# Optimization experiments

Hardware: AMD Instinct MI355X
Metric: run time of the kernel (lower is better)

Reference implementation:

```python
import jax, jax.numpy as jnp
import numpy as np

N_NODES = 50000
NB = 32          # neighbor-list width per metapath
NFEAT = 128
NHID = 64
DIM_MP = 64
EDIM = 32
NMETA = 3
NCLASS = 8
B = 10000
ALPHA = 0.2


def setup_inputs() -> dict:
    key = jax.random.key(0)
    ks = jax.random.split(key, 16)
    s = 0.05
    return {
        "input": jax.random.normal(ks[0], (B, NFEAT), jnp.float32),
        "index": jax.random.randint(ks[1], (B,), 0, N_NODES),
        "node_emb": jax.random.normal(ks[2], (N_NODES, NFEAT), jnp.float32),
        "edge_index": jax.random.randint(ks[3], (NMETA, N_NODES, NB), 0, N_NODES, dtype=jnp.int32),
        "edge_emb": jax.random.normal(ks[4], (NMETA, N_NODES * NB, EDIM), jnp.float32) * 0.1,
        "n_sample": 32,
        "Wq1": jax.random.normal(ks[5], (NMETA, NFEAT, NHID), jnp.float32) * s,
        "Wk1": jax.random.normal(ks[6], (NMETA, NFEAT, NHID), jnp.float32) * s,
        "a1": jax.random.normal(ks[7], (NMETA, 2 * NHID + EDIM), jnp.float32) * s,
        "Wq2": jax.random.normal(ks[8], (NMETA, NHID, DIM_MP), jnp.float32) * s,
        "Wk2": jax.random.normal(ks[9], (NMETA, NFEAT, DIM_MP), jnp.float32) * s,
        "a2": jax.random.normal(ks[10], (NMETA, 2 * DIM_MP + EDIM), jnp.float32) * s,
        "a_mp": jax.random.normal(ks[11], (DIM_MP,), jnp.float32) * s,
        "Wc": jax.random.normal(ks[12], (DIM_MP, NCLASS), jnp.float32) * s,
        "bc": jnp.zeros((NCLASS,), jnp.float32),
    }


def _aggr(x, index, node_emb, nbr_tab, e_tab, Wq, Wk, a, out_dim, n_sample):
    """GAT-style edge-embedding attention aggregation over sampled neighbors.
    x:[B,in]  nbr_tab:[N,NB] int  e_tab:[N,NB,E]
    """
    nbrs = nbr_tab[index][:, :n_sample]              # [B,S] gathered neighbor ids
    e_emb = e_tab[index][:, :n_sample]               # [B,S,E] per-edge embeddings
    hq = x @ Wq                                      # [B,out]
    hk = node_emb[nbrs] @ Wk                         # [B,S,out] (irregular gather + GEMM)
    # attention score: a^T [hq || hk || e_ij]
    scores = (hq @ a[:out_dim])[:, None] + hk @ a[out_dim:2 * out_dim] + e_emb @ a[2 * out_dim:]
    scores = jax.nn.leaky_relu(scores, ALPHA)        # [B,S]
    att = jax.nn.softmax(scores, axis=1)
    agg = jnp.einsum('bs,bso->bo', att, hk)          # scatter-weighted aggregation
    return jax.nn.elu(agg)


def reference(input, index, node_emb, edge_index, edge_emb,
              Wq1, Wk1, a1, Wq2, Wk2, a2, a_mp, Wc, bc, n_sample):
    embs = []
    for m in range(NMETA):  # fixed small metapath loop (structurally distinct params)
        nbr_tab = edge_index[m]                              # [N,NB]
        e_tab = edge_emb[m].reshape(N_NODES, NB, EDIM)       # [N,NB,E]
        x1 = _aggr(input, index, node_emb, nbr_tab, e_tab, Wq1[m], Wk1[m], a1[m], NHID, n_sample)
        x2 = _aggr(x1, index, node_emb, nbr_tab, e_tab, Wq2[m], Wk2[m], a2[m], DIM_MP, n_sample)
        embs.append(x2)
    emb = jnp.stack(embs)                                    # [M,B,R]
    # metapath-level attention fusion
    e = jax.nn.leaky_relu(emb @ a_mp, ALPHA)                 # [M,B]
    att = jax.nn.softmax(e, axis=0)
    fused = jnp.einsum('mb,mbr->br', att, emb)               # [B,R]
    logits = jax.nn.relu(fused @ Wc + bc)                    # [B,nclass]
    return jax.nn.log_softmax(logits, axis=1)
```

## Files before the change

### kernel.cpp

```cpp
#include <hip/hip_runtime.h>
#include <hip/hip_bf16.h>
#include <cstddef>

#define NNODES 50000
#define NBW    32
#define NFEAT  128
#define NHID   64
#define EDIM   32
#define NMETA  3
#define NCLASS 8
#define BB     10000
#define SS     32

#define OFF_HKA   9600000
#define OFF_WQ1V  9900000
#define OFF_WQ2V  9900384
#define OFF_WBF   9900576

#define NGEMMBLK  782

typedef __attribute__((ext_vector_type(8))) short bf16x8;
typedef __attribute__((ext_vector_type(4))) float f32x4;

static __device__ __forceinline__ unsigned short f2bf(float x) {
    unsigned u = __float_as_uint(x);
    return (unsigned short)((u + 0x7fffu + ((u >> 16) & 1u)) >> 16);
}
static __device__ __forceinline__ float rdlane_f(float v, int l) {
    return __int_as_float(__builtin_amdgcn_readlane(__float_as_int(v), l));
}

__global__ void prep_kernel(const float* __restrict__ Wq1, const float* __restrict__ a1,
                            const float* __restrict__ Wq2, const float* __restrict__ a2,
                            const float* __restrict__ Wk1, const float* __restrict__ Wk2,
                            float* __restrict__ wq1v, float* __restrict__ wq2v,
                            unsigned short* __restrict__ Bf)
{
    int blk = blockIdx.x, t = threadIdx.x;
    if (blk < 24) {
        int id = blk * 256 + t;
        int lane = id & 63;
        int t4 = (id >> 6) & 3;
        int kk = (id >> 8) & 3;
        int mat = id >> 10;
        const float* W = (mat < 3) ? (Wk1 + (size_t)mat * 8192)
                                   : (Wk2 + (size_t)(mat - 3) * 8192);
        int c  = t4 * 16 + (lane & 15);
        int kb = kk * 32 + (lane >> 4) * 8;
        unsigned short* dst = Bf + (size_t)id * 8;
        #pragma unroll
        for (int j = 0; j < 8; ++j) dst[j] = f2bf(W[(size_t)(kb + j) * 64 + c]);
    } else {
        int m = blk - 24;
        if (t < 128) {
            float acc = 0.f;
            const float* w = Wq1 + (m * 128 + t) * 64;
            const float* a = a1 + m * 160;
            #pragma unroll 8
            for (int c = 0; c < 64; ++c) acc += w[c] * a[c];
            wq1v[m * 128 + t] = acc;
        } else if (t < 192) {
            int f = t - 128;
            float acc = 0.f;
            const float* w = Wq2 + (m * 64 + f) * 64;
            const float* a = a2 + m * 160;
            #pragma unroll 8
            for (int c = 0; c < 64; ++c) acc += w[c] * a[c];
            wq2v[m * 64 + f] = acc;
        }
    }
}

__global__ __launch_bounds__(256) void hk_mfma6(const float* __restrict__ node_emb,
                                                const unsigned short* __restrict__ Bf,
                                                const float* __restrict__ a1,
                                                const float* __restrict__ a2,
                                                unsigned* __restrict__ HKI,
                                                float* __restrict__ hkaI)
{
    __shared__ char lds_a[64 * 256];
    int nbase = blockIdx.x * 64;
    int t = threadIdx.x;

    #pragma unroll
    for (int i = 0; i < 8; ++i) {
        int fi = (i * 256 + t) * 4;
        int row = fi >> 7, k0 = fi & 127;
        int gn = nbase + row;
        float4 v = (gn < NNODES) ? *(const float4*)(node_emb + (size_t)gn * 128 + k0)
                                 : float4{0.f, 0.f, 0.f, 0.f};
        unsigned lo = (unsigned)f2bf(v.x) | ((unsigned)f2bf(v.y) << 16);
        unsigned hi = (unsigned)f2bf(v.z) | ((unsigned)f2bf(v.w) << 16);
        int byte = (row * 256 + k0 * 2) ^ ((row & 7) << 4);
        *(uint2*)(lds_a + byte) = uint2{lo, hi};
    }
    __syncthreads();

    int w = t >> 6, lane = t & 63;
    int row_l = lane & 15, kgrp = lane >> 4;
    int row = w * 16 + row_l;

    bf16x8 afr[4];
    #pragma unroll
    for (int kk = 0; kk < 4; ++kk) {
        int byte = (row * 256 + kk * 64 + kgrp * 16) ^ ((row_l & 7) << 4);
        afr[kk] = *(const bf16x8*)(lds_a + byte);
    }

    int col0 = lane & 15;
    #pragma unroll
    for (int mm = 0; mm < 3; ++mm) {
        f32x4 acc0[4], acc1[4];
        #pragma unroll
        for (int j = 0; j < 4; ++j) { acc0[j] = f32x4{0,0,0,0}; acc1[j] = f32x4{0,0,0,0}; }
        #pragma unroll
        for (int kk = 0; kk < 4; ++kk) {
            #pragma unroll
            for (int t4 = 0; t4 < 4; ++t4) {
                bf16x8 b0 = *(const bf16x8*)(Bf + ((size_t)((mm * 4 + kk) * 4 + t4) * 64 + lane) * 8);
                bf16x8 b1 = *(const bf16x8*)(Bf + ((size_t)(((3 + mm) * 4 + kk) * 4 + t4) * 64 + lane) * 8);
                acc0[t4] = __builtin_amdgcn_mfma_f32_16x16x32_bf16(afr[kk], b0, acc0[t4], 0, 0, 0);
                acc1[t4] = __builtin_amdgcn_mfma_f32_16x16x32_bf16(afr[kk], b1, acc1[t4], 0, 0, 0);
            }
        }
        const float* ak0 = a1 + mm * 160 + 64;
        const float* ak1 = a2 + mm * 160 + 64;
        float akv0[4], akv1[4];
        #pragma unroll
        for (int t4 = 0; t4 < 4; ++t4) { akv0[t4] = ak0[t4 * 16 + col0]; akv1[t4] = ak1[t4 * 16 + col0]; }
        #pragma unroll
        for (int r = 0; r < 4; ++r) {
            int n = nbase + w * 16 + kgrp * 4 + r;
            float hp0 = acc0[0][r] * akv0[0] + acc0[1][r] * akv0[1]
                      + acc0[2][r] * akv0[2] + acc0[3][r] * akv0[3];
            float hp1 = acc1[0][r] * akv1[0] + acc1[1][r] * akv1[1]
                      + acc1[2][r] * akv1[2] + acc1[3][r] * akv1[3];
            #pragma unroll
            for (int off = 8; off; off >>= 1) {
                hp0 += __shfl_xor(hp0, off, 16);
                hp1 += __shfl_xor(hp1, off, 16);
            }
            if (n < NNODES) {
                unsigned* dst = HKI + ((size_t)mm * NNODES + n) * 64;
                #pragma unroll
                for (int t4 = 0; t4 < 4; ++t4)
                    dst[t4 * 16 + col0] = (unsigned)f2bf(acc0[t4][r])
                                        | ((unsigned)f2bf(acc1[t4][r]) << 16);
                if (col0 == 0)
                    *(float2*)(hkaI + ((size_t)mm * NNODES + n) * 2) = float2{hp0, hp1};
            }
        }
    }
}

__global__ __launch_bounds__(192, 5) void fused_kernel(const float* __restrict__ input,
                                                    const int* __restrict__ index,
                                                    const int* __restrict__ edge_index,
                                                    const float* __restrict__ edge_emb,
                                                    const unsigned* __restrict__ HKI,
                                                    const float* __restrict__ hkaI,
                                                    const float* __restrict__ wq1v,
                                                    const float* __restrict__ wq2v,
                                                    const float* __restrict__ a1,
                                                    const float* __restrict__ a2,
                                                    const float* __restrict__ a_mp,
                                                    const float* __restrict__ Wc,
                                                    const float* __restrict__ bc,
                                                    float* __restrict__ out)
{
    __shared__ float s_e[3][32][33];
    __shared__ float s_att[3][32];
    __shared__ float s_ed1[3][32];
    __shared__ float s_emb[3][64];
    __shared__ float s_sc[3];

    int t = threadIdx.x, lane = t & 63;
    int m = __builtin_amdgcn_readfirstlane(t >> 6);
    int w = m;
    int b = blockIdx.x;
    int idx = __builtin_amdgcn_readfirstlane(index[b]);
    int s = lane & 31;

    const int* eidx = edge_index + ((size_t)m * NNODES + idx) * NBW;
    int nbr_l = eidx[s];

    const float4* src = (const float4*)(edge_emb + ((size_t)m * NNODES + idx) * (NBW * EDIM));
    float4 ef[4];
    #pragma unroll
    for (int i = 0; i < 4; ++i) ef[i] = src[i * 64 + lane];

    float2 ha = *(const float2*)(hkaI + ((size_t)m * NNODES + nbr_l) * 2);

    const unsigned* TAB = HKI + (size_t)m * NNODES * 64;
    unsigned h[32];
    #pragma unroll
    for (int j = 0; j < 32; ++j) {
        int nj = eidx[j];
        h[j] = TAB[(size_t)nj * 64 + lane];
    }

    #pragma unroll
    for (int i = 0; i < 4; ++i) {
        int li = i * 64 + lane;
        int r = li >> 3, c4 = (li & 7) * 4;
        s_e[w][r][c4]     = ef[i].x;
        s_e[w][r][c4 + 1] = ef[i].y;
        s_e[w][r][c4 + 2] = ef[i].z;
        s_e[w][r][c4 + 3] = ef[i].w;
    }

    int lvl = lane >> 5;
    const float* ae = (lvl ? a2 : a1) + m * 160 + 128;
    float ed = 0.f;
    #pragma unroll
    for (int k = 0; k < 32; ++k) ed += s_e[w][s][k] * ae[k];
    if (lvl) s_ed1[w][s] = ed;

    float hv = input[(size_t)b * 128 + lane] * wq1v[m * 128 + lane]
             + input[(size_t)b * 128 + 64 + lane] * wq1v[m * 128 + 64 + lane];
    #pragma unroll
    for (int off = 32; off; off >>= 1) hv += __shfl_xor(hv, off, 64);

    if (lane < 32) {
        float sc = hv + ha.x + ed;
        sc = sc > 0.f ? sc : 0.2f * sc;
        float mx = sc;
        #pragma unroll
        for (int off = 16; off; off >>= 1) mx = fmaxf(mx, __shfl_xor(mx, off, 32));
        float p = expf(sc - mx);
        float sm = p;
        #pragma unroll
        for (int off = 16; off; off >>= 1) sm += __shfl_xor(sm, off, 32);
        s_att[w][lane] = p / sm;
    }

    float acc = 0.f;
    #pragma unroll
    for (int j = 0; j < 32; ++j)
        acc += s_att[w][j] * __uint_as_float(h[j] << 16);
    float x = acc > 0.f ? acc : expm1f(acc);

    float hv2 = x * wq2v[m * 64 + lane];
    #pragma unroll
    for (int off = 32; off; off >>= 1) hv2 += __shfl_xor(hv2, off, 64);

    if (lane < 32) {
        float sc = hv2 + ha.y + s_ed1[w][lane];
        sc = sc > 0.f ? sc : 0.2f * sc;
        float mx = sc;
        #pragma unroll
        for (int off = 16; off; off >>= 1) mx = fmaxf(mx, __shfl_xor(mx, off, 32));
        float p = expf(sc - mx);
        float sm = p;
        #pragma unroll
        for (int off = 16; off; off >>= 1) sm += __shfl_xor(sm, off, 32);
        s_att[w][lane] = p / sm;
    }

    acc = 0.f;
    #pragma unroll
    for (int j = 0; j < 32; ++j)
        acc += s_att[w][j] * __uint_as_float(h[j] & 0xffff0000u);
    float emb_c = acc > 0.f ? acc : expm1f(acc);
    s_emb[w][lane] = emb_c;

    float ev = emb_c * a_mp[lane];
    #pragma unroll
    for (int off = 32; off; off >>= 1) ev += __shfl_xor(ev, off, 64);
    if (lane == 0) s_sc[w] = ev > 0.f ? ev : 0.2f * ev;
    __syncthreads();

    if (w == 0) {
        float e0 = s_sc[0], e1 = s_sc[1], e2 = s_sc[2];
        float mx3 = fmaxf(e0, fmaxf(e1, e2));
        float p0 = expf(e0 - mx3), p1 = expf(e1 - mx3), p2 = expf(e2 - mx3);
        float sminv = 1.f / (p0 + p1 + p2);

        int g = lane >> 3, r = lane & 7;
        float v = 0.f;
        #pragma unroll
        for (int k = 0; k < 8; ++k) {
            int c = r + 8 * k;
            float fc = (p0 * s_emb[0][c] + p1 * s_emb[1][c] + p2 * s_emb[2][c]) * sminv;
            v += fc * Wc[c * NCLASS + g];
        }
        v += __shfl_xor(v, 1, 64);
        v += __shfl_xor(v, 2, 64);
        v += __shfl_xor(v, 4, 64);
        float lg = fmaxf(v + bc[g], 0.f);

        float l0 = rdlane_f(lg, 0),  l1 = rdlane_f(lg, 8),  l2 = rdlane_f(lg, 16), l3 = rdlane_f(lg, 24);
        float l4 = rdlane_f(lg, 32), l5 = rdlane_f(lg, 40), l6 = rdlane_f(lg, 48), l7 = rdlane_f(lg, 56);
        float m8 = fmaxf(fmaxf(fmaxf(l0, l1), fmaxf(l2, l3)),
                         fmaxf(fmaxf(l4, l5), fmaxf(l6, l7)));
        float se = expf(l0 - m8) + expf(l1 - m8) + expf(l2 - m8) + expf(l3 - m8)
                 + expf(l4 - m8) + expf(l5 - m8) + expf(l6 - m8) + expf(l7 - m8);
        float ls = logf(se);
        if (lane < 8) {
            float lj = lane == 0 ? l0 : lane == 1 ? l1 : lane == 2 ? l2 : lane == 3 ? l3
                     : lane == 4 ? l4 : lane == 5 ? l5 : lane == 6 ? l6 : l7;
            out[(size_t)b * NCLASS + lane] = lj - m8 - ls;
        }
    }
}

extern "C" void kernel_launch(void* const* d_in, const int* in_sizes, int n_in,
                              void* d_out, int out_size, void* d_ws, size_t ws_size,
                              hipStream_t stream)
{
    const float* input     = (const float*)d_in[0];
    const int*   index     = (const int*)d_in[1];
    const float* node_emb  = (const float*)d_in[2];
    const int*   edge_index= (const int*)d_in[3];
    const float* edge_emb  = (const float*)d_in[4];
    const float* Wq1 = (const float*)d_in[6];
    const float* Wk1 = (const float*)d_in[7];
    const float* a1  = (const float*)d_in[8];
    const float* Wq2 = (const float*)d_in[9];
    const float* Wk2 = (const float*)d_in[10];
    const float* a2  = (const float*)d_in[11];
    const float* a_mp= (const float*)d_in[12];
    const float* Wc  = (const float*)d_in[13];
    const float* bc  = (const float*)d_in[14];

    float* ws = (float*)d_ws;
    unsigned* HKI = (unsigned*)d_ws;
    float* hkaI = ws + OFF_HKA;
    float* wq1v = ws + OFF_WQ1V;
    float* wq2v = ws + OFF_WQ2V;
    unsigned short* Bf = (unsigned short*)(ws + OFF_WBF);

    prep_kernel<<<dim3(27), dim3(256), 0, stream>>>(Wq1, a1, Wq2, a2, Wk1, Wk2,
                                                    wq1v, wq2v, Bf);
    hk_mfma6<<<dim3(NGEMMBLK), dim3(256), 0, stream>>>(
        node_emb, Bf, a1, a2, HKI, hkaI);
    fused_kernel<<<dim3(BB), dim3(192), 0, stream>>>(
        input, index, edge_index, edge_emb, HKI, hkaI, wq1v, wq2v,
        a1, a2, a_mp, Wc, bc, (float*)d_out);
}
```

Baseline: 94.30 us.

## Precompute edge-embedding attention dots in mid kernel alongside hk GEMM

Moves the per-edge dot product of edge embeddings with the attention vectors out of the fused kernel into extra blocks of the middle kernel, which now runs them alongside the GEMM blocks. The fused kernel reads a compact 64-float row per (metapath, batch) instead of 4KB of edge embeddings, and it no longer needs the LDS transpose buffer. This is meant to cut register and LDS pressure and the load latency in the fused kernel, and to overlap the edge streaming with the GEMM. In exchange it adds a workspace round trip of the dot results and more blocks in the middle launch.

```diff
diff --git a/kernel.cpp b/kernel.cpp
--- a/kernel.cpp
+++ b/kernel.cpp
@@ -16,8 +16,10 @@
 #define OFF_WQ1V  9900000
 #define OFF_WQ2V  9900384
 #define OFF_WBF   9900576
+#define OFF_EDOT  9925152
 
 #define NGEMMBLK  782
+#define NEDOTBLK  7500
 
 typedef __attribute__((ext_vector_type(8))) short bf16x8;
 typedef __attribute__((ext_vector_type(4))) float f32x4;
@@ -71,16 +73,42 @@
     }
 }
 
-__global__ __launch_bounds__(256) void hk_mfma6(const float* __restrict__ node_emb,
-                                                const unsigned short* __restrict__ Bf,
-                                                const float* __restrict__ a1,
-                                                const float* __restrict__ a2,
-                                                unsigned* __restrict__ HKI,
-                                                float* __restrict__ hkaI)
+__global__ __launch_bounds__(256) void mid_kernel(const float* __restrict__ node_emb,
+                                                  const unsigned short* __restrict__ Bf,
+                                                  const float* __restrict__ a1,
+                                                  const float* __restrict__ a2,
+                                                  const int* __restrict__ index,
+                                                  const float* __restrict__ edge_emb,
+                                                  unsigned* __restrict__ HKI,
+                                                  float* __restrict__ hkaI,
+                                                  float* __restrict__ edotw)
 {
     __shared__ char lds_a[64 * 256];
-    int nbase = blockIdx.x * 64;
+    int bid = blockIdx.x;
     int t = threadIdx.x;
+
+    if (bid >= NGEMMBLK) {
+        int eb = bid - NGEMMBLK;
+        int w = t >> 6, lane = t & 63;
+        int m = eb / (BB / 4);
+        int b = (eb % (BB / 4)) * 4 + w;
+        int idx = index[b];
+        int s = lane & 31, lvl = lane >> 5;
+        const float4* rowp = (const float4*)(edge_emb + ((size_t)m * NNODES + idx) * (NBW * EDIM))
+                           + s * 8;
+        const float* ae = (lvl ? a2 : a1) + m * 160 + 128;
+        float ed = 0.f;
+        #pragma unroll
+        for (int i = 0; i < 8; ++i) {
+            float4 e4 = rowp[i];
+            float4 a4 = *(const float4*)(ae + i * 4);
+            ed += e4.x * a4.x + e4.y * a4.y + e4.z * a4.z + e4.w * a4.w;
+        }
+        edotw[((size_t)m * BB + b) * 64 + lane] = ed;
+        return;
+    }
+
+    int nbase = bid * 64;
 
     #pragma unroll
     for (int i = 0; i < 8; ++i) {
@@ -156,19 +184,16 @@
 __global__ __launch_bounds__(192, 5) void fused_kernel(const float* __restrict__ input,
                                                     const int* __restrict__ index,
                                                     const int* __restrict__ edge_index,
-                                                    const float* __restrict__ edge_emb,
+                                                    const float* __restrict__ edotw,
                                                     const unsigned* __restrict__ HKI,
                                                     const float* __restrict__ hkaI,
                                                     const float* __restrict__ wq1v,
                                                     const float* __restrict__ wq2v,
-                                                    const float* __restrict__ a1,
-                                                    const float* __restrict__ a2,
                                                     const float* __restrict__ a_mp,
                                                     const float* __restrict__ Wc,
                                                     const float* __restrict__ bc,
                                                     float* __restrict__ out)
 {
-    __shared__ float s_e[3][32][33];
     __shared__ float s_att[3][32];
     __shared__ float s_ed1[3][32];
     __shared__ float s_emb[3][64];
@@ -184,10 +209,8 @@
     const int* eidx = edge_index + ((size_t)m * NNODES + idx) * NBW;
     int nbr_l = eidx[s];
 
-    const float4* src = (const float4*)(edge_emb + ((size_t)m * NNODES + idx) * (NBW * EDIM));
-    float4 ef[4];
-    #pragma unroll
-    for (int i = 0; i < 4; ++i) ef[i] = src[i * 64 + lane];
+    float ed = edotw[((size_t)m * BB + b) * 64 + lane];
+    if (lane >= 32) s_ed1[w][lane - 32] = ed;
 
     float2 ha = *(const float2*)(hkaI + ((size_t)m * NNODES + nbr_l) * 2);
 
@@ -198,23 +221,6 @@
         int nj = eidx[j];
         h[j] = TAB[(size_t)nj * 64 + lane];
     }
-
-    #pragma unroll
-    for (int i = 0; i < 4; ++i) {
-        int li = i * 64 + lane;
-        int r = li >> 3, c4 = (li & 7) * 4;
-        s_e[w][r][c4]     = ef[i].x;
-        s_e[w][r][c4 + 1] = ef[i].y;
-        s_e[w][r][c4 + 2] = ef[i].z;
-        s_e[w][r][c4 + 3] = ef[i].w;
-    }
-
-    int lvl = lane >> 5;
-    const float* ae = (lvl ? a2 : a1) + m * 160 + 128;
-    float ed = 0.f;
-    #pragma unroll
-    for (int k = 0; k < 32; ++k) ed += s_e[w][s][k] * ae[k];
-    if (lvl) s_ed1[w][s] = ed;
 
     float hv = input[(size_t)b * 128 + lane] * wq1v[m * 128 + lane]
              + input[(size_t)b * 128 + 64 + lane] * wq1v[m * 128 + 64 + lane];
@@ -329,12 +335,13 @@
     float* wq1v = ws + OFF_WQ1V;
     float* wq2v = ws + OFF_WQ2V;
     unsigned short* Bf = (unsigned short*)(ws + OFF_WBF);
+    float* edotw = ws + OFF_EDOT;
 
     prep_kernel<<<dim3(27), dim3(256), 0, stream>>>(Wq1, a1, Wq2, a2, Wk1, Wk2,
                                                     wq1v, wq2v, Bf);
-    hk_mfma6<<<dim3(NGEMMBLK), dim3(256), 0, stream>>>(
-        node_emb, Bf, a1, a2, HKI, hkaI);
+    mid_kernel<<<dim3(NGEMMBLK + NEDOTBLK), dim3(256), 0, stream>>>(
+        node_emb, Bf, a1, a2, index, edge_emb, HKI, hkaI, edotw);
     fused_kernel<<<dim3(BB), dim3(192), 0, stream>>>(
-        input, index, edge_index, edge_emb, HKI, hkaI, wq1v, wq2v,
-        a1, a2, a_mp, Wc, bc, (float*)d_out);
-}
+        input, index, edge_index, edotw, HKI, hkaI, wq1v, wq2v,
+        a_mp, Wc, bc, (float*)d_out);
+}
```

After: 103.6 us. 9.9% more time.
